# Optimization experiments

Measured on AMD Instinct MI355X. Metric: run time of the kernel, lower is better.

The kernel has to match this reference:

```python
import jax, jax.numpy as jnp
import numpy as np

# Dims: tokens [B,H,W,C]; 3x3 local window (NB=9 neighbors); relative-pos embed dim RP.
B, H, W, C = 4, 96, 96, 128
K, NB, RP = 3, 9, 8
HID = 128              # edge_hidden_dim = max(hidden_dim//2=128, feature_dim=128)
EDGE_IN = 3 * C + RP   # [center, neighbor, center-neighbor, rel_pos] -> 392
CLIP = 3.0
GATE_EPS = 1e-6
LN_EPS = 1e-5


def _ln(x, w, b):
    m = jnp.mean(x, axis=-1, keepdims=True)
    v = jnp.mean((x - m) ** 2, axis=-1, keepdims=True)
    return (x - m) * jax.lax.rsqrt(v + LN_EPS) * w + b


def _mlp(x, w1, b1, w2, b2):
    # Linear -> GELU (exact/erf, torch default) -> Linear; dropout is identity in eval mode.
    return jax.nn.gelu(x @ w1 + b1, approximate=False) @ w2 + b2


def _eml(drive, resistance, gamma_raw, lam, bias, warmup_eta):
    # EMLUnit energy gate (source not provided; Ohm's-law style drive/resistance,
    # positive resistance via softplus, clipped, warmup-scaled, learned bias).
    gamma = jax.nn.softplus(gamma_raw)
    conduct = drive / (jax.nn.softplus(resistance) + gamma + GATE_EPS)
    return warmup_eta * jnp.clip(lam * conduct, -CLIP, CLIP) + bias


def setup_inputs() -> dict:
    key = jax.random.key(0)
    ks = jax.random.split(key, 8)

    def w(k, shape, std=0.01):
        return jax.random.normal(k, shape, jnp.float32) * std

    return {
        "tokens": jax.random.normal(ks[0], (B, H, W, C), jnp.float32),
        "ln1_w": jnp.ones((C,), jnp.float32), "ln1_b": jnp.zeros((C,), jnp.float32),
        "ln2_w": jnp.ones((C,), jnp.float32), "ln2_b": jnp.zeros((C,), jnp.float32),
        "rel_pos": w(ks[1], (NB, RP), 0.02),
        "d_w1": w(ks[2], (EDGE_IN, HID)), "d_b1": jnp.zeros((HID,), jnp.float32),
        "d_w2": w(ks[3], (HID, 1)), "d_b2": jnp.zeros((1,), jnp.float32),
        "r_w1": w(ks[4], (EDGE_IN, HID)), "r_b1": jnp.zeros((HID,), jnp.float32),
        "r_w2": w(ks[5], (HID, 1)), "r_b2": jnp.zeros((1,), jnp.float32),
        "v_w": w(ks[6], (C, C)), "v_b": jnp.zeros((C,), jnp.float32),
        "o_w": w(ks[7], (C, C)), "o_b": jnp.zeros((C,), jnp.float32),
        "eml_gamma": jnp.full((1,), 0.1, jnp.float32),
        "eml_lam": jnp.ones((1,), jnp.float32),
        "eml_bias": jnp.full((1,), -0.3, jnp.float32),
    }


def reference(tokens, ln1_w, ln1_b, ln2_w, ln2_b, rel_pos,
              d_w1, d_b1, d_w2, d_b2, r_w1, r_b1, r_w2, r_b2,
              v_w, v_b, o_w, o_b, eml_gamma, eml_lam, eml_bias):
    b, h, w_, c = tokens.shape
    hw = h * w_
    norm = _ln(tokens, ln1_w, ln1_b)
    # nn.Unfold(kernel=3, padding=1): zero-pad then gather 3x3 windows (row-major ky,kx order).
    pad = jnp.pad(norm, ((0, 0), (1, 1), (1, 1), (0, 0)))
    neigh = jnp.stack([pad[:, dy:dy + h, dx:dx + w_, :]
                       for dy in range(K) for dx in range(K)], axis=3)  # [B,H,W,9,C]
    neigh = neigh.reshape(b, hw, NB, c)
    center = jnp.broadcast_to(norm.reshape(b, hw, 1, c), (b, hw, NB, c))
    relp = jnp.broadcast_to(rel_pos[None, None], (b, hw, NB, RP))
    edge = jnp.concatenate([center, neigh, center - neigh, relp], axis=-1)  # [B,HW,9,392]
    drive = _mlp(edge, d_w1, d_b1, d_w2, d_b2)[..., 0]        # [B,HW,9]
    resistance = _mlp(edge, r_w1, r_b1, r_w2, r_b2)[..., 0]   # [B,HW,9]
    energy = _eml(drive, resistance, eml_gamma, eml_lam, eml_bias, 1.0)
    gate = jax.nn.sigmoid(energy)[..., None]                  # [B,HW,9,1]
    values = neigh @ v_w + v_b                                # [B,HW,9,C]
    gate_mass = jnp.clip(jnp.sum(gate, axis=2), GATE_EPS, None)  # [B,HW,1]
    message = jnp.sum(gate * values, axis=2) / gate_mass      # [B,HW,C]
    update = (message @ o_w + o_b).reshape(b, h, w_, c)
    return _ln(tokens + update, ln2_w, ln2_b)
```

## Files before the change

### kernel.cpp

```cpp
#include <hip/hip_runtime.h>
#include <stdint.h>

#define NPIX 36864

using bf16x8 = __attribute__((ext_vector_type(8))) short;
using f32x4  = __attribute__((ext_vector_type(4))) float;
using f32x2  = __attribute__((ext_vector_type(2))) float;

__device__ __forceinline__ float bf2f(uint16_t u){
  return __uint_as_float(((uint32_t)u) << 16);
}
__device__ __forceinline__ float bl(uint32_t u){ return __uint_as_float(u << 16); }
__device__ __forceinline__ float bh(uint32_t u){ return __uint_as_float(u & 0xFFFF0000u); }
__device__ __forceinline__ uint16_t f2bf(float f){
  uint32_t u = __float_as_uint(f);
  u += 0x7fffu + ((u >> 16) & 1u);
  return (uint16_t)(u >> 16);
}
__device__ __forceinline__ float ldw(const void* p, int i, bool f32){
  return f32 ? ((const float*)p)[i] : bf2f(((const uint16_t*)p)[i]);
}
__device__ __forceinline__ bool probe_f32(const void* ones_vec){
  return ((const uint32_t*)ones_vec)[0] == 0x3F800000u;
}
__device__ __forceinline__ float softplusf(float x){
  return fmaxf(x, 0.f) + __logf(1.f + __expf(-fabsf(x)));
}
__device__ __forceinline__ f32x2 up2(uint32_t u){
  f32x2 r; r.x = __uint_as_float(u << 16); r.y = __uint_as_float(u & 0xFFFF0000u); return r;
}
__device__ __forceinline__ void sg2(f32x2& acc, uint32_t c, uint32_t n, f32x2 r, f32x2 w){
  f32x2 z = up2(c) + up2(n) + r;
  f32x2 t = z * (-1.702f);
  f32x2 e; e.x = __expf(t.x); e.y = __expf(t.y);
  f32x2 den = e + 1.0f;
  f32x2 s; s.x = __builtin_amdgcn_rcpf(den.x); s.y = __builtin_amdgcn_rcpf(den.y);
  acc += z * s * w;
}

__global__ __launch_bounds__(256) void pre_kernel(const void* __restrict__ tokens,
                            const void* __restrict__ ln1w, const void* __restrict__ ln1b,
                            const void* __restrict__ dw1, const void* __restrict__ rw1,
                            const void* __restrict__ vw,  const void* __restrict__ relp,
                            const void* __restrict__ db1, const void* __restrict__ rb1,
                            const void* __restrict__ ow,
                            const void* __restrict__ dw2, const void* __restrict__ rw2,
                            const void* __restrict__ vb,  const void* __restrict__ db2,
                            const void* __restrict__ rb2, const void* __restrict__ eg,
                            const void* __restrict__ el,  const void* __restrict__ eb,
                            uint16_t* __restrict__ norm,
                            uint16_t* __restrict__ wcatT, float* __restrict__ Rd,
                            float* __restrict__ Rr, uint16_t* __restrict__ owT,
                            float* __restrict__ w2df, float* __restrict__ w2rf,
                            float* __restrict__ vbf, float* __restrict__ sc){
  const bool F = probe_f32(ln1w);
  const int b = blockIdx.x;
  if (b < NPIX/4){
    const int wv = threadIdx.x >> 6, lane = threadIdx.x & 63;
    const int p = b * 4 + wv;
    float f0, f1;
    if (F){
      const float2 t = ((const float2*)tokens)[(size_t)p*64 + lane];
      f0 = t.x; f1 = t.y;
    } else {
      const uint32_t pk = ((const uint32_t*)tokens)[(size_t)p*64 + lane];
      f0 = bl(pk); f1 = bh(pk);
    }
    float s = f0 + f1;
    #pragma unroll
    for (int m = 1; m < 64; m <<= 1) s += __shfl_xor(s, m, 64);
    const float mean = s * (1.f/128.f);
    const float d0 = f0 - mean, d1 = f1 - mean;
    float q = d0*d0 + d1*d1;
    #pragma unroll
    for (int m = 1; m < 64; m <<= 1) q += __shfl_xor(q, m, 64);
    const float rs = rsqrtf(q * (1.f/128.f) + 1e-5f);
    const float n0 = d0*rs*ldw(ln1w, 2*lane, F)   + ldw(ln1b, 2*lane, F);
    const float n1 = d1*rs*ldw(ln1w, 2*lane+1, F) + ldw(ln1b, 2*lane+1, F);
    ((uint32_t*)(norm + (size_t)p*128))[lane] = (uint32_t)f2bf(n0) | ((uint32_t)f2bf(n1) << 16);
    return;
  }
  const int j = (b - NPIX/4) * 2 + (threadIdx.x >> 7);
  const int c = threadIdx.x & 127;
  if (j < 640){
    float val;
    if (j < 128)      val = ldw(dw1, c*128 + j, F)             + ldw(dw1, (256+c)*128 + j, F);
    else if (j < 256) val = ldw(dw1, (128+c)*128 + (j-128), F) - ldw(dw1, (256+c)*128 + (j-128), F);
    else if (j < 384) val = ldw(rw1, c*128 + (j-256), F)       + ldw(rw1, (256+c)*128 + (j-256), F);
    else if (j < 512) val = ldw(rw1, (128+c)*128 + (j-384), F) - ldw(rw1, (256+c)*128 + (j-384), F);
    else              val = ldw(vw, c*128 + (j-512), F);
    wcatT[j*128 + c] = f2bf(val);
  } else if (j < 649){
    const int k = j - 640;
    float sd = ldw(db1, c, F);
    float sr = ldw(rb1, c, F);
    #pragma unroll
    for (int r = 0; r < 8; ++r){
      float rp = ldw(relp, k*8 + r, F);
      sd += rp * ldw(dw1, (384+r)*128 + c, F);
      sr += rp * ldw(rw1, (384+r)*128 + c, F);
    }
    Rd[k*128 + c] = sd;
    Rr[k*128 + c] = sr;
  } else if (j < 777){
    const int n = j - 649;
    owT[n*128 + c] = f2bf(ldw(ow, c*128 + n, F));
  } else {
    w2df[c] = ldw(dw2, c, F);
    w2rf[c] = ldw(rw2, c, F);
    vbf[c]  = ldw(vb, c, F);
    if (c == 0){
      sc[0] = ldw(db2, 0, F);
      sc[1] = ldw(rb2, 0, F);
      sc[2] = softplusf(ldw(eg, 0, F));
      sc[3] = ldw(el, 0, F);
      sc[4] = ldw(eb, 0, F);
    }
  }
}

#define CSTRIDE 136
__global__ __launch_bounds__(256) void gemm1_kernel(const uint16_t* __restrict__ A,
                                                    const uint16_t* __restrict__ BT,
                                                    uint16_t* __restrict__ PT,
                                                    uint16_t* __restrict__ V){
  __shared__ __align__(16) char smem[65536];
  uint16_t* As = (uint16_t*)smem;
  uint16_t* Bs = (uint16_t*)(smem + 32768);
  uint16_t* Cs = (uint16_t*)smem;
  const int row0 = blockIdx.x * 128;
  const int s    = blockIdx.y;
  const int col0 = s * 128;
  const int t = threadIdx.x;
  #pragma unroll
  for (int i = 0; i < 8; ++i){
    int cid = t + i*256;
    int r = cid >> 4, c8 = cid & 15;
    int scz = c8 ^ (r & 15);
    *(uint4*)&As[r*128 + scz*8] = *(const uint4*)&A[(size_t)(row0+r)*128 + c8*8];
    *(uint4*)&Bs[r*128 + scz*8] = *(const uint4*)&BT[(size_t)(col0+r)*128 + c8*8];
  }
  __syncthreads();
  const int wv = t >> 6, lane = t & 63;
  const int wr = (wv >> 1) * 64, wc = (wv & 1) * 64;
  const int lr = lane & 15, quad = lane >> 4;
  f32x4 acc[4][4] = {};
  #pragma unroll
  for (int kk = 0; kk < 4; ++kk){
    const int chunk = kk*4 + quad;
    bf16x8 a[4], b[4];
    #pragma unroll
    for (int mi = 0; mi < 4; ++mi){
      int r = wr + mi*16 + lr;
      a[mi] = *(const bf16x8*)&As[r*128 + (chunk ^ (r & 15))*8];
    }
    #pragma unroll
    for (int ni = 0; ni < 4; ++ni){
      int r = wc + ni*16 + lr;
      b[ni] = *(const bf16x8*)&Bs[r*128 + (chunk ^ (r & 15))*8];
    }
    #pragma unroll
    for (int mi = 0; mi < 4; ++mi)
      #pragma unroll
      for (int ni = 0; ni < 4; ++ni)
        acc[mi][ni] = __builtin_amdgcn_mfma_f32_16x16x32_bf16(a[mi], b[ni], acc[mi][ni], 0, 0, 0);
  }
  __syncthreads();
  #pragma unroll
  for (int mi = 0; mi < 4; ++mi){
    #pragma unroll
    for (int ni = 0; ni < 4; ++ni){
      const int ch   = wc + ni*16 + lr;
      const int rowb = wr + mi*16 + quad*4;
      #pragma unroll
      for (int r = 0; r < 4; ++r)
        Cs[(rowb + r)*CSTRIDE + ch] = f2bf(acc[mi][ni][r]);
    }
  }
  __syncthreads();
  if (s < 4){
    #pragma unroll
    for (int i = 0; i < 8; ++i){
      const int idx = t + i*256;
      const int p = idx & 127, c = idx >> 7;
      const uint4 v = *(const uint4*)&Cs[p*CSTRIDE + c*8];
      ((uint4*)PT)[(size_t)(s*16 + c)*NPIX + (row0 + p)] = v;
    }
  } else {
    #pragma unroll
    for (int i = 0; i < 8; ++i){
      const int idx = t + i*256;
      const int c8 = idx & 15, p = idx >> 4;
      const uint4 v = *(const uint4*)&Cs[p*CSTRIDE + c8*8];
      ((uint4*)V)[(size_t)(row0 + p)*16 + c8] = v;
    }
  }
}

__global__ __launch_bounds__(192) void edge_kernel(const uint16_t* __restrict__ PTraw,
    const float* __restrict__ Rd, const float* __restrict__ Rr,
    const float* __restrict__ w2df, const float* __restrict__ w2rf,
    const float* __restrict__ sc, float* __restrict__ gates){
  const int wv = threadIdx.x >> 6, lane = threadIdx.x & 63;
  const int k = __builtin_amdgcn_readfirstlane(blockIdx.y * 3 + wv);
  const int p = blockIdx.x * 64 + lane;
  const int dy = k/3 - 1, dx = k%3 - 1;
  const int x = p % 96, y = (p / 96) % 96;
  const bool inb = ((unsigned)(x + dx) < 96u) && ((unsigned)(y + dy) < 96u);
  const uint32_t m = inb ? 0xFFFFFFFFu : 0u;
  const int q = inb ? (p + dy*96 + dx) : p;
  const uint4* PT4 = (const uint4*)PTraw;
  const float4* rd4 = (const float4*)(Rd + k*128);
  const float4* rr4 = (const float4*)(Rr + k*128);
  const float4* wd4 = (const float4*)w2df;
  const float4* wr4 = (const float4*)w2rf;
  const float sc0 = sc[0], sc1 = sc[1], sc2 = sc[2], sc3 = sc[3], sc4 = sc[4];
  f32x2 ad = {0.f, 0.f}, ar = {0.f, 0.f};
  uint4 cd = PT4[(size_t)( 0)*NPIX + p];
  uint4 nd = PT4[(size_t)(16)*NPIX + q];
  uint4 cr = PT4[(size_t)(32)*NPIX + p];
  uint4 nr = PT4[(size_t)(48)*NPIX + q];
  #pragma unroll
  for (int i = 0; i < 16; ++i){
    uint4 cdn, ndn, crn, nrn;
    if (i < 15){
      cdn = PT4[(size_t)( 0 + i+1)*NPIX + p];
      ndn = PT4[(size_t)(16 + i+1)*NPIX + q];
      crn = PT4[(size_t)(32 + i+1)*NPIX + p];
      nrn = PT4[(size_t)(48 + i+1)*NPIX + q];
    }
    nd.x &= m; nd.y &= m; nd.z &= m; nd.w &= m;
    nr.x &= m; nr.y &= m; nr.z &= m; nr.w &= m;
    const float4 rdA = rd4[2*i], rdB = rd4[2*i+1];
    const float4 rrA = rr4[2*i], rrB = rr4[2*i+1];
    const float4 wdA = wd4[2*i], wdB = wd4[2*i+1];
    const float4 wrA = wr4[2*i], wrB = wr4[2*i+1];
    sg2(ad, cd.x, nd.x, f32x2{rdA.x, rdA.y}, f32x2{wdA.x, wdA.y});
    sg2(ad, cd.y, nd.y, f32x2{rdA.z, rdA.w}, f32x2{wdA.z, wdA.w});
    sg2(ad, cd.z, nd.z, f32x2{rdB.x, rdB.y}, f32x2{wdB.x, wdB.y});
    sg2(ad, cd.w, nd.w, f32x2{rdB.z, rdB.w}, f32x2{wdB.z, wdB.w});
    sg2(ar, cr.x, nr.x, f32x2{rrA.x, rrA.y}, f32x2{wrA.x, wrA.y});
    sg2(ar, cr.y, nr.y, f32x2{rrA.z, rrA.w}, f32x2{wrA.z, wrA.w});
    sg2(ar, cr.z, nr.z, f32x2{rrB.x, rrB.y}, f32x2{wrB.x, wrB.y});
    sg2(ar, cr.w, nr.w, f32x2{rrB.z, rrB.w}, f32x2{wrB.z, wrB.w});
    cd = cdn; nd = ndn; cr = crn; nr = nrn;
  }
  const float drive  = (ad.x + ad.y) + sc0;
  const float resist = (ar.x + ar.y) + sc1;
  const float cond = __fdividef(drive, softplusf(resist) + sc2 + 1e-6f);
  const float en = fminf(fmaxf(sc3 * cond, -3.0f), 3.0f) + sc4;
  const float e = __expf(-en);
  const float g = __builtin_amdgcn_rcpf(1.0f + e);
  gates[(size_t)k*NPIX + p] = g;
}

__global__ __launch_bounds__(256) void msg_kernel(const uint16_t* __restrict__ V,
    const float* __restrict__ gates, const float* __restrict__ vbf,
    uint16_t* __restrict__ msg){
  const int wv = __builtin_amdgcn_readfirstlane(threadIdx.x >> 6);
  const int lane = threadIdx.x & 63;
  const int p = blockIdx.x * 4 + wv;
  const int x = p % 96, y = (p / 96) % 96;
  float g[9], gsum = 0.f;
  #pragma unroll
  for (int k = 0; k < 9; ++k){ g[k] = gates[(size_t)k*NPIX + p]; gsum += g[k]; }
  float a0 = 0.f, a1 = 0.f;
  #pragma unroll
  for (int k = 0; k < 9; ++k){
    const int dy = k/3 - 1, dx = k%3 - 1;
    if (((unsigned)(y + dy) < 96u) && ((unsigned)(x + dx) < 96u)){
      const uint32_t u = ((const uint32_t*)(V + (size_t)(p + dy*96 + dx)*128))[lane];
      a0 = fmaf(g[k], bl(u), a0);
      a1 = fmaf(g[k], bh(u), a1);
    }
  }
  const float2 vb2 = ((const float2*)vbf)[lane];
  const float inv = __fdividef(1.0f, fmaxf(gsum, 1e-6f));
  a0 = (a0 + gsum * vb2.x) * inv;
  a1 = (a1 + gsum * vb2.y) * inv;
  ((uint32_t*)(msg + (size_t)p*128))[lane] = (uint32_t)f2bf(a0) | ((uint32_t)f2bf(a1) << 16);
}

__global__ __launch_bounds__(256) void out_kernel(const uint16_t* __restrict__ Amsg,
    const uint16_t* __restrict__ owT, const void* __restrict__ tokens,
    const void* __restrict__ ob,  const void* __restrict__ ln2w,
    const void* __restrict__ ln2b, void* __restrict__ out){
  const bool F = probe_f32(ln2w);
  __shared__ __align__(16) char smem[65536];
  uint16_t* As = (uint16_t*)smem;
  uint16_t* Bs = (uint16_t*)(smem + 32768);
  float*    U  = (float*)smem;
  const int row0 = blockIdx.x * 128;
  const int t = threadIdx.x;
  #pragma unroll
  for (int i = 0; i < 8; ++i){
    int cid = t + i*256;
    int r = cid >> 4, c8 = cid & 15;
    int scz = c8 ^ (r & 15);
    *(uint4*)&As[r*128 + scz*8] = *(const uint4*)&Amsg[(size_t)(row0+r)*128 + c8*8];
    *(uint4*)&Bs[r*128 + scz*8] = *(const uint4*)&owT[(size_t)r*128 + c8*8];
  }
  __syncthreads();
  const int wv = t >> 6, lane = t & 63;
  const int wr = (wv >> 1) * 64, wc = (wv & 1) * 64;
  const int lr = lane & 15, quad = lane >> 4;
  f32x4 acc[4][4] = {};
  #pragma unroll
  for (int kk = 0; kk < 4; ++kk){
    const int chunk = kk*4 + quad;
    bf16x8 a[4], b[4];
    #pragma unroll
    for (int mi = 0; mi < 4; ++mi){
      int r = wr + mi*16 + lr;
      a[mi] = *(const bf16x8*)&As[r*128 + (chunk ^ (r & 15))*8];
    }
    #pragma unroll
    for (int ni = 0; ni < 4; ++ni){
      int r = wc + ni*16 + lr;
      b[ni] = *(const bf16x8*)&Bs[r*128 + (chunk ^ (r & 15))*8];
    }
    #pragma unroll
    for (int mi = 0; mi < 4; ++mi)
      #pragma unroll
      for (int ni = 0; ni < 4; ++ni)
        acc[mi][ni] = __builtin_amdgcn_mfma_f32_16x16x32_bf16(a[mi], b[ni], acc[mi][ni], 0, 0, 0);
  }
  __syncthreads();
  #pragma unroll
  for (int mi = 0; mi < 4; ++mi)
    #pragma unroll
    for (int ni = 0; ni < 4; ++ni)
      #pragma unroll
      for (int r = 0; r < 4; ++r)
        U[(wr + mi*16 + quad*4 + r)*128 + (wc + ni*16 + lr)] = acc[mi][ni][r];
  __syncthreads();
  const float lw0 = ldw(ln2w, 2*lane, F), lw1 = ldw(ln2w, 2*lane+1, F);
  const float lb0 = ldw(ln2b, 2*lane, F), lb1 = ldw(ln2b, 2*lane+1, F);
  const float ob0 = ldw(ob, 2*lane, F),   ob1 = ldw(ob, 2*lane+1, F);
  for (int rr = 0; rr < 32; ++rr){
    const int row = wv*32 + rr;
    const int p = row0 + row;
    const float2 uv = ((const float2*)U)[row*64 + lane];
    float t0, t1;
    if (F){
      const float2 tk = ((const float2*)tokens)[(size_t)p*64 + lane];
      t0 = tk.x; t1 = tk.y;
    } else {
      const uint32_t tk = ((const uint32_t*)tokens)[(size_t)p*64 + lane];
      t0 = bl(tk); t1 = bh(tk);
    }
    const float a0 = uv.x + ob0 + t0;
    const float a1 = uv.y + ob1 + t1;
    float s = a0 + a1;
    #pragma unroll
    for (int m = 1; m < 64; m <<= 1) s += __shfl_xor(s, m, 64);
    const float mean = s * (1.f/128.f);
    const float d0 = a0 - mean, d1 = a1 - mean;
    float q = d0*d0 + d1*d1;
    #pragma unroll
    for (int m = 1; m < 64; m <<= 1) q += __shfl_xor(q, m, 64);
    const float rs = rsqrtf(q * (1.f/128.f) + 1e-5f);
    const float o0 = d0*rs*lw0 + lb0;
    const float o1 = d1*rs*lw1 + lb1;
    if (F){
      ((float2*)out)[(size_t)p*64 + lane] = make_float2(o0, o1);
    } else {
      ((uint32_t*)out)[(size_t)p*64 + lane] = (uint32_t)f2bf(o0) | ((uint32_t)f2bf(o1) << 16);
    }
  }
}

extern "C" void kernel_launch(void* const* d_in, const int* in_sizes, int n_in,
                              void* d_out, int out_size, void* d_ws, size_t ws_size,
                              hipStream_t stream) {
  const void* tokens = d_in[0];
  const void* ln1w   = d_in[1];
  const void* ln1b   = d_in[2];
  const void* ln2w   = d_in[3];
  const void* ln2b   = d_in[4];
  const void* relp   = d_in[5];
  const void* dw1    = d_in[6];
  const void* db1    = d_in[7];
  const void* dw2    = d_in[8];
  const void* db2    = d_in[9];
  const void* rw1    = d_in[10];
  const void* rb1    = d_in[11];
  const void* rw2    = d_in[12];
  const void* rb2    = d_in[13];
  const void* vw     = d_in[14];
  const void* vb     = d_in[15];
  const void* ow     = d_in[16];
  const void* ob     = d_in[17];
  const void* eg     = d_in[18];
  const void* el     = d_in[19];
  const void* eb     = d_in[20];

  char* ws = (char*)d_ws;
  uint16_t* normb = (uint16_t*)(ws + 0);
  uint16_t* PT    = (uint16_t*)(ws + 9437184);
  uint16_t* V     = (uint16_t*)(ws + 47185920);
  float*    gates = (float*)   (ws + 56623104);
  uint16_t* wcatT = (uint16_t*)(ws + 57950208);
  float*    Rd    = (float*)   (ws + 58114048);
  float*    Rr    = (float*)   (ws + 58118656);
  uint16_t* owT   = (uint16_t*)(ws + 58123264);
  float*    w2df  = (float*)   (ws + 58156032);
  float*    w2rf  = (float*)   (ws + 58156544);
  float*    vbf   = (float*)   (ws + 58157056);
  float*    sc    = (float*)   (ws + 58157568);
  uint16_t* msg   = normb;

  pre_kernel<<<NPIX/4 + 389, 256, 0, stream>>>(tokens, ln1w, ln1b,
                                       dw1, rw1, vw, relp, db1, rb1, ow,
                                       dw2, rw2, vb, db2, rb2, eg, el, eb,
                                       normb, wcatT, Rd, Rr, owT, w2df, w2rf, vbf, sc);
  gemm1_kernel<<<dim3(NPIX/128, 5), 256, 0, stream>>>(normb, wcatT, PT, V);
  edge_kernel<<<dim3(NPIX/64, 3), 192, 0, stream>>>(PT, Rd, Rr, w2df, w2rf, sc, gates);
  msg_kernel<<<NPIX/4, 256, 0, stream>>>(V, gates, vbf, msg);
  out_kernel<<<NPIX/128, 256, 0, stream>>>(msg, owT, tokens, ob, ln2w, ln2b, d_out);
}
```

Baseline: 210.3 us.

## Fuse LayerNorm into edge GEMM, fuse message gather into output GEMM

LayerNorm-1 now runs inside the first GEMM kernel, which writes normalized rows straight to shared memory and then loops over all five weight column slabs, instead of storing `norm` to global memory. The message gather is folded into the output GEMM kernel the same way, so `msg` never goes through global memory and two kernel launches disappear. The sigmoid-based GELU approximation is also swapped for an algebraic rsqrt form, with the 0.5 factor folded into the second-layer weights. In exchange, both fused kernels launch only 288 blocks and each wave processes 32 pixels one after another, which lowers parallelism and latency hiding.

```diff
diff --git a/kernel.cpp b/kernel.cpp
--- a/kernel.cpp
+++ b/kernel.cpp
@@ -31,56 +31,33 @@
 }
 __device__ __forceinline__ void sg2(f32x2& acc, uint32_t c, uint32_t n, f32x2 r, f32x2 w){
   f32x2 z = up2(c) + up2(n) + r;
-  f32x2 t = z * (-1.702f);
-  f32x2 e; e.x = __expf(t.x); e.y = __expf(t.y);
-  f32x2 den = e + 1.0f;
-  f32x2 s; s.x = __builtin_amdgcn_rcpf(den.x); s.y = __builtin_amdgcn_rcpf(den.y);
-  acc += z * s * w;
-}
-
-__global__ __launch_bounds__(256) void pre_kernel(const void* __restrict__ tokens,
-                            const void* __restrict__ ln1w, const void* __restrict__ ln1b,
+  f32x2 t = z * 0.851f;
+  float rsx = rsqrtf(fmaf(t.x, t.x, 1.0f));
+  float rsy = rsqrtf(fmaf(t.y, t.y, 1.0f));
+  f32x2 zt = z * t;
+  float gx = fmaf(zt.x, rsx, z.x);
+  float gy = fmaf(zt.y, rsy, z.y);
+  acc.x = fmaf(gx, w.x, acc.x);
+  acc.y = fmaf(gy, w.y, acc.y);
+}
+
+#define LIDX(p, ch) ((p)*128 + ((((ch) >> 3) ^ ((p) & 15)) << 3) + ((ch) & 7))
+
+__global__ __launch_bounds__(256) void pre_kernel(
                             const void* __restrict__ dw1, const void* __restrict__ rw1,
                             const void* __restrict__ vw,  const void* __restrict__ relp,
                             const void* __restrict__ db1, const void* __restrict__ rb1,
-                            const void* __restrict__ ow,
+                            const void* __restrict__ ow,  const void* __restrict__ probe,
                             const void* __restrict__ dw2, const void* __restrict__ rw2,
                             const void* __restrict__ vb,  const void* __restrict__ db2,
                             const void* __restrict__ rb2, const void* __restrict__ eg,
                             const void* __restrict__ el,  const void* __restrict__ eb,
-                            uint16_t* __restrict__ norm,
                             uint16_t* __restrict__ wcatT, float* __restrict__ Rd,
                             float* __restrict__ Rr, uint16_t* __restrict__ owT,
                             float* __restrict__ w2df, float* __restrict__ w2rf,
                             float* __restrict__ vbf, float* __restrict__ sc){
-  const bool F = probe_f32(ln1w);
-  const int b = blockIdx.x;
-  if (b < NPIX/4){
-    const int wv = threadIdx.x >> 6, lane = threadIdx.x & 63;
-    const int p = b * 4 + wv;
-    float f0, f1;
-    if (F){
-      const float2 t = ((const float2*)tokens)[(size_t)p*64 + lane];
-      f0 = t.x; f1 = t.y;
-    } else {
-      const uint32_t pk = ((const uint32_t*)tokens)[(size_t)p*64 + lane];
-      f0 = bl(pk); f1 = bh(pk);
-    }
-    float s = f0 + f1;
-    #pragma unroll
-    for (int m = 1; m < 64; m <<= 1) s += __shfl_xor(s, m, 64);
-    const float mean = s * (1.f/128.f);
-    const float d0 = f0 - mean, d1 = f1 - mean;
-    float q = d0*d0 + d1*d1;
-    #pragma unroll
-    for (int m = 1; m < 64; m <<= 1) q += __shfl_xor(q, m, 64);
-    const float rs = rsqrtf(q * (1.f/128.f) + 1e-5f);
-    const float n0 = d0*rs*ldw(ln1w, 2*lane, F)   + ldw(ln1b, 2*lane, F);
-    const float n1 = d1*rs*ldw(ln1w, 2*lane+1, F) + ldw(ln1b, 2*lane+1, F);
-    ((uint32_t*)(norm + (size_t)p*128))[lane] = (uint32_t)f2bf(n0) | ((uint32_t)f2bf(n1) << 16);
-    return;
-  }
-  const int j = (b - NPIX/4) * 2 + (threadIdx.x >> 7);
+  const bool F = probe_f32(probe);
+  const int j = blockIdx.x * 2 + (threadIdx.x >> 7);
   const int c = threadIdx.x & 127;
   if (j < 640){
     float val;
@@ -106,8 +83,8 @@
     const int n = j - 649;
     owT[n*128 + c] = f2bf(ldw(ow, c*128 + n, F));
   } else {
-    w2df[c] = ldw(dw2, c, F);
-    w2rf[c] = ldw(rw2, c, F);
+    w2df[c] = 0.5f * ldw(dw2, c, F);
+    w2rf[c] = 0.5f * ldw(rw2, c, F);
     vbf[c]  = ldw(vb, c, F);
     if (c == 0){
       sc[0] = ldw(db2, 0, F);
@@ -119,81 +96,106 @@
   }
 }
 
-#define CSTRIDE 136
-__global__ __launch_bounds__(256) void gemm1_kernel(const uint16_t* __restrict__ A,
-                                                    const uint16_t* __restrict__ BT,
-                                                    uint16_t* __restrict__ PT,
-                                                    uint16_t* __restrict__ V){
+__global__ __launch_bounds__(256) void gemmln_kernel(const void* __restrict__ tokens,
+    const void* __restrict__ ln1w, const void* __restrict__ ln1b,
+    const uint16_t* __restrict__ BT, uint16_t* __restrict__ PT, uint16_t* __restrict__ V){
+  const bool F = probe_f32(ln1w);
   __shared__ __align__(16) char smem[65536];
   uint16_t* As = (uint16_t*)smem;
   uint16_t* Bs = (uint16_t*)(smem + 32768);
-  uint16_t* Cs = (uint16_t*)smem;
   const int row0 = blockIdx.x * 128;
-  const int s    = blockIdx.y;
-  const int col0 = s * 128;
   const int t = threadIdx.x;
-  #pragma unroll
-  for (int i = 0; i < 8; ++i){
-    int cid = t + i*256;
-    int r = cid >> 4, c8 = cid & 15;
-    int scz = c8 ^ (r & 15);
-    *(uint4*)&As[r*128 + scz*8] = *(const uint4*)&A[(size_t)(row0+r)*128 + c8*8];
-    *(uint4*)&Bs[r*128 + scz*8] = *(const uint4*)&BT[(size_t)(col0+r)*128 + c8*8];
-  }
-  __syncthreads();
   const int wv = t >> 6, lane = t & 63;
+  {
+    const float w0 = ldw(ln1w, 2*lane, F), w1 = ldw(ln1w, 2*lane+1, F);
+    const float b0 = ldw(ln1b, 2*lane, F), b1 = ldw(ln1b, 2*lane+1, F);
+    for (int j = 0; j < 32; ++j){
+      const int pl = wv*32 + j;
+      const int p = row0 + pl;
+      float f0, f1;
+      if (F){
+        const float2 tk = ((const float2*)tokens)[(size_t)p*64 + lane];
+        f0 = tk.x; f1 = tk.y;
+      } else {
+        const uint32_t pk = ((const uint32_t*)tokens)[(size_t)p*64 + lane];
+        f0 = bl(pk); f1 = bh(pk);
+      }
+      float s = f0 + f1;
+      #pragma unroll
+      for (int m = 1; m < 64; m <<= 1) s += __shfl_xor(s, m, 64);
+      const float mean = s * (1.f/128.f);
+      const float d0 = f0 - mean, d1 = f1 - mean;
+      float q = d0*d0 + d1*d1;
+      #pragma unroll
+      for (int m = 1; m < 64; m <<= 1) q += __shfl_xor(q, m, 64);
+      const float rs = rsqrtf(q * (1.f/128.f) + 1e-5f);
+      const float n0 = d0*rs*w0 + b0;
+      const float n1 = d1*rs*w1 + b1;
+      *(uint32_t*)&As[LIDX(pl, 2*lane)] = (uint32_t)f2bf(n0) | ((uint32_t)f2bf(n1) << 16);
+    }
+  }
   const int wr = (wv >> 1) * 64, wc = (wv & 1) * 64;
   const int lr = lane & 15, quad = lane >> 4;
-  f32x4 acc[4][4] = {};
-  #pragma unroll
-  for (int kk = 0; kk < 4; ++kk){
-    const int chunk = kk*4 + quad;
-    bf16x8 a[4], b[4];
+  for (int s = 0; s < 5; ++s){
+    #pragma unroll
+    for (int i = 0; i < 8; ++i){
+      const int cid = t + i*256;
+      const int r = cid >> 4, c8 = cid & 15;
+      *(uint4*)&Bs[r*128 + ((c8 ^ (r & 15)) << 3)] = *(const uint4*)&BT[(size_t)(s*128 + r)*128 + c8*8];
+    }
+    __syncthreads();
+    f32x4 acc[4][4] = {};
+    #pragma unroll
+    for (int kk = 0; kk < 4; ++kk){
+      const int chunk = kk*4 + quad;
+      bf16x8 a[4], b[4];
+      #pragma unroll
+      for (int mi = 0; mi < 4; ++mi){
+        const int r = wr + mi*16 + lr;
+        a[mi] = *(const bf16x8*)&As[r*128 + ((chunk ^ (r & 15)) << 3)];
+      }
+      #pragma unroll
+      for (int ni = 0; ni < 4; ++ni){
+        const int r = wc + ni*16 + lr;
+        b[ni] = *(const bf16x8*)&Bs[r*128 + ((chunk ^ (r & 15)) << 3)];
+      }
+      #pragma unroll
+      for (int mi = 0; mi < 4; ++mi)
+        #pragma unroll
+        for (int ni = 0; ni < 4; ++ni)
+          acc[mi][ni] = __builtin_amdgcn_mfma_f32_16x16x32_bf16(a[mi], b[ni], acc[mi][ni], 0, 0, 0);
+    }
+    __syncthreads();
     #pragma unroll
     for (int mi = 0; mi < 4; ++mi){
-      int r = wr + mi*16 + lr;
-      a[mi] = *(const bf16x8*)&As[r*128 + (chunk ^ (r & 15))*8];
-    }
-    #pragma unroll
-    for (int ni = 0; ni < 4; ++ni){
-      int r = wc + ni*16 + lr;
-      b[ni] = *(const bf16x8*)&Bs[r*128 + (chunk ^ (r & 15))*8];
-    }
-    #pragma unroll
-    for (int mi = 0; mi < 4; ++mi)
-      #pragma unroll
-      for (int ni = 0; ni < 4; ++ni)
-        acc[mi][ni] = __builtin_amdgcn_mfma_f32_16x16x32_bf16(a[mi], b[ni], acc[mi][ni], 0, 0, 0);
-  }
-  __syncthreads();
-  #pragma unroll
-  for (int mi = 0; mi < 4; ++mi){
-    #pragma unroll
-    for (int ni = 0; ni < 4; ++ni){
-      const int ch   = wc + ni*16 + lr;
-      const int rowb = wr + mi*16 + quad*4;
-      #pragma unroll
-      for (int r = 0; r < 4; ++r)
-        Cs[(rowb + r)*CSTRIDE + ch] = f2bf(acc[mi][ni][r]);
-    }
-  }
-  __syncthreads();
-  if (s < 4){
-    #pragma unroll
-    for (int i = 0; i < 8; ++i){
-      const int idx = t + i*256;
-      const int p = idx & 127, c = idx >> 7;
-      const uint4 v = *(const uint4*)&Cs[p*CSTRIDE + c*8];
-      ((uint4*)PT)[(size_t)(s*16 + c)*NPIX + (row0 + p)] = v;
-    }
-  } else {
-    #pragma unroll
-    for (int i = 0; i < 8; ++i){
-      const int idx = t + i*256;
-      const int c8 = idx & 15, p = idx >> 4;
-      const uint4 v = *(const uint4*)&Cs[p*CSTRIDE + c8*8];
-      ((uint4*)V)[(size_t)(row0 + p)*16 + c8] = v;
-    }
+      #pragma unroll
+      for (int ni = 0; ni < 4; ++ni){
+        const int ch = wc + ni*16 + lr;
+        const int rowb = wr + mi*16 + quad*4;
+        #pragma unroll
+        for (int r = 0; r < 4; ++r)
+          Bs[LIDX(rowb + r, ch)] = f2bf(acc[mi][ni][r]);
+      }
+    }
+    __syncthreads();
+    if (s < 4){
+      #pragma unroll
+      for (int i = 0; i < 8; ++i){
+        const int idx = t + i*256;
+        const int p = idx & 127, c = idx >> 7;
+        const uint4 v = *(const uint4*)&Bs[p*128 + ((c ^ (p & 15)) << 3)];
+        ((uint4*)PT)[(size_t)(s*16 + c)*NPIX + (row0 + p)] = v;
+      }
+    } else {
+      #pragma unroll
+      for (int i = 0; i < 8; ++i){
+        const int idx = t + i*256;
+        const int c8 = idx & 15, p = idx >> 4;
+        const uint4 v = *(const uint4*)&Bs[p*128 + ((c8 ^ (p & 15)) << 3)];
+        ((uint4*)V)[(size_t)(row0 + p)*16 + c8] = v;
+      }
+    }
+    __syncthreads();
   }
 }
 
@@ -254,36 +256,10 @@
   gates[(size_t)k*NPIX + p] = g;
 }
 
-__global__ __launch_bounds__(256) void msg_kernel(const uint16_t* __restrict__ V,
+__global__ __launch_bounds__(256) void msgout_kernel(const uint16_t* __restrict__ V,
     const float* __restrict__ gates, const float* __restrict__ vbf,
-    uint16_t* __restrict__ msg){
-  const int wv = __builtin_amdgcn_readfirstlane(threadIdx.x >> 6);
-  const int lane = threadIdx.x & 63;
-  const int p = blockIdx.x * 4 + wv;
-  const int x = p % 96, y = (p / 96) % 96;
-  float g[9], gsum = 0.f;
-  #pragma unroll
-  for (int k = 0; k < 9; ++k){ g[k] = gates[(size_t)k*NPIX + p]; gsum += g[k]; }
-  float a0 = 0.f, a1 = 0.f;
-  #pragma unroll
-  for (int k = 0; k < 9; ++k){
-    const int dy = k/3 - 1, dx = k%3 - 1;
-    if (((unsigned)(y + dy) < 96u) && ((unsigned)(x + dx) < 96u)){
-      const uint32_t u = ((const uint32_t*)(V + (size_t)(p + dy*96 + dx)*128))[lane];
-      a0 = fmaf(g[k], bl(u), a0);
-      a1 = fmaf(g[k], bh(u), a1);
-    }
-  }
-  const float2 vb2 = ((const float2*)vbf)[lane];
-  const float inv = __fdividef(1.0f, fmaxf(gsum, 1e-6f));
-  a0 = (a0 + gsum * vb2.x) * inv;
-  a1 = (a1 + gsum * vb2.y) * inv;
-  ((uint32_t*)(msg + (size_t)p*128))[lane] = (uint32_t)f2bf(a0) | ((uint32_t)f2bf(a1) << 16);
-}
-
-__global__ __launch_bounds__(256) void out_kernel(const uint16_t* __restrict__ Amsg,
     const uint16_t* __restrict__ owT, const void* __restrict__ tokens,
-    const void* __restrict__ ob,  const void* __restrict__ ln2w,
+    const void* __restrict__ ob, const void* __restrict__ ln2w,
     const void* __restrict__ ln2b, void* __restrict__ out){
   const bool F = probe_f32(ln2w);
   __shared__ __align__(16) char smem[65536];
@@ -292,16 +268,39 @@
   float*    U  = (float*)smem;
   const int row0 = blockIdx.x * 128;
   const int t = threadIdx.x;
+  const int wv = t >> 6, lane = t & 63;
   #pragma unroll
   for (int i = 0; i < 8; ++i){
-    int cid = t + i*256;
-    int r = cid >> 4, c8 = cid & 15;
-    int scz = c8 ^ (r & 15);
-    *(uint4*)&As[r*128 + scz*8] = *(const uint4*)&Amsg[(size_t)(row0+r)*128 + c8*8];
-    *(uint4*)&Bs[r*128 + scz*8] = *(const uint4*)&owT[(size_t)r*128 + c8*8];
+    const int cid = t + i*256;
+    const int r = cid >> 4, c8 = cid & 15;
+    *(uint4*)&Bs[r*128 + ((c8 ^ (r & 15)) << 3)] = *(const uint4*)&owT[(size_t)r*128 + c8*8];
+  }
+  {
+    const float2 vb2 = ((const float2*)vbf)[lane];
+    for (int j = 0; j < 32; ++j){
+      const int pl = wv*32 + j;
+      const int p = row0 + pl;
+      const int x = p % 96, y = (p / 96) % 96;
+      float g[9], gsum = 0.f;
+      #pragma unroll
+      for (int k = 0; k < 9; ++k){ g[k] = gates[(size_t)k*NPIX + p]; gsum += g[k]; }
+      float a0 = 0.f, a1 = 0.f;
+      #pragma unroll
+      for (int k = 0; k < 9; ++k){
+        const int dy = k/3 - 1, dx = k%3 - 1;
+        if (((unsigned)(y + dy) < 96u) && ((unsigned)(x + dx) < 96u)){
+          const uint32_t u = ((const uint32_t*)V)[(size_t)(p + dy*96 + dx)*64 + lane];
+          a0 = fmaf(g[k], bl(u), a0);
+          a1 = fmaf(g[k], bh(u), a1);
+        }
+      }
+      const float inv = __fdividef(1.0f, fmaxf(gsum, 1e-6f));
+      a0 = (a0 + gsum * vb2.x) * inv;
+      a1 = (a1 + gsum * vb2.y) * inv;
+      *(uint32_t*)&As[LIDX(pl, 2*lane)] = (uint32_t)f2bf(a0) | ((uint32_t)f2bf(a1) << 16);
+    }
   }
   __syncthreads();
-  const int wv = t >> 6, lane = t & 63;
   const int wr = (wv >> 1) * 64, wc = (wv & 1) * 64;
   const int lr = lane & 15, quad = lane >> 4;
   f32x4 acc[4][4] = {};
@@ -311,13 +310,13 @@
     bf16x8 a[4], b[4];
     #pragma unroll
     for (int mi = 0; mi < 4; ++mi){
-      int r = wr + mi*16 + lr;
-      a[mi] = *(const bf16x8*)&As[r*128 + (chunk ^ (r & 15))*8];
+      const int r = wr + mi*16 + lr;
+      a[mi] = *(const bf16x8*)&As[r*128 + ((chunk ^ (r & 15)) << 3)];
     }
     #pragma unroll
     for (int ni = 0; ni < 4; ++ni){
-      int r = wc + ni*16 + lr;
-      b[ni] = *(const bf16x8*)&Bs[r*128 + (chunk ^ (r & 15))*8];
+      const int r = wc + ni*16 + lr;
+      b[ni] = *(const bf16x8*)&Bs[r*128 + ((chunk ^ (r & 15)) << 3)];
     }
     #pragma unroll
     for (int mi = 0; mi < 4; ++mi)
@@ -396,26 +395,22 @@
   const void* eb     = d_in[20];
 
   char* ws = (char*)d_ws;
-  uint16_t* normb = (uint16_t*)(ws + 0);
-  uint16_t* PT    = (uint16_t*)(ws + 9437184);
-  uint16_t* V     = (uint16_t*)(ws + 47185920);
-  float*    gates = (float*)   (ws + 56623104);
-  uint16_t* wcatT = (uint16_t*)(ws + 57950208);
-  float*    Rd    = (float*)   (ws + 58114048);
-  float*    Rr    = (float*)   (ws + 58118656);
-  uint16_t* owT   = (uint16_t*)(ws + 58123264);
-  float*    w2df  = (float*)   (ws + 58156032);
-  float*    w2rf  = (float*)   (ws + 58156544);
-  float*    vbf   = (float*)   (ws + 58157056);
-  float*    sc    = (float*)   (ws + 58157568);
-  uint16_t* msg   = normb;
-
-  pre_kernel<<<NPIX/4 + 389, 256, 0, stream>>>(tokens, ln1w, ln1b,
-                                       dw1, rw1, vw, relp, db1, rb1, ow,
-                                       dw2, rw2, vb, db2, rb2, eg, el, eb,
-                                       normb, wcatT, Rd, Rr, owT, w2df, w2rf, vbf, sc);
-  gemm1_kernel<<<dim3(NPIX/128, 5), 256, 0, stream>>>(normb, wcatT, PT, V);
+  uint16_t* PT    = (uint16_t*)(ws + 0);
+  uint16_t* V     = (uint16_t*)(ws + 37748736);
+  float*    gates = (float*)   (ws + 47185920);
+  uint16_t* wcatT = (uint16_t*)(ws + 48513024);
+  float*    Rd    = (float*)   (ws + 48676864);
+  float*    Rr    = (float*)   (ws + 48681472);
+  uint16_t* owT   = (uint16_t*)(ws + 48686080);
+  float*    w2df  = (float*)   (ws + 48718848);
+  float*    w2rf  = (float*)   (ws + 48719360);
+  float*    vbf   = (float*)   (ws + 48719872);
+  float*    sc    = (float*)   (ws + 48720384);
+
+  pre_kernel<<<389, 256, 0, stream>>>(dw1, rw1, vw, relp, db1, rb1, ow, ln1w,
+                                      dw2, rw2, vb, db2, rb2, eg, el, eb,
+                                      wcatT, Rd, Rr, owT, w2df, w2rf, vbf, sc);
+  gemmln_kernel<<<NPIX/128, 256, 0, stream>>>(tokens, ln1w, ln1b, wcatT, PT, V);
   edge_kernel<<<dim3(NPIX/64, 3), 192, 0, stream>>>(PT, Rd, Rr, w2df, w2rf, sc, gates);
-  msg_kernel<<<NPIX/4, 256, 0, stream>>>(V, gates, vbf, msg);
-  out_kernel<<<NPIX/128, 256, 0, stream>>>(msg, owT, tokens, ob, ln2w, ln2b, d_out);
-}
+  msgout_kernel<<<NPIX/128, 256, 0, stream>>>(V, gates, vbf, owT, tokens, ob, ln2w, ln2b, d_out);
+}
```

New measurement: 404.5 us. 1.92x slower.

## Fuse gated message aggregation into the output projection and LayerNorm kernel

Applied to the files above, without the earlier changes.

Merges msg_kernel and out_kernel into one kernel. Each block computes the gated neighbor messages for 64 pixels directly into swizzled LDS, then runs the 128x128 output projection with MFMA and the residual+LayerNorm epilogue. This drops a kernel launch and the global round trip of the bf16 message tensor. In exchange each block reloads the full owT weight, and the tile is smaller (64 rows, one wave per 16 rows), so there is less MFMA reuse per block.

```diff
diff --git a/kernel.cpp b/kernel.cpp
--- a/kernel.cpp
+++ b/kernel.cpp
@@ -37,6 +37,8 @@
   f32x2 s; s.x = __builtin_amdgcn_rcpf(den.x); s.y = __builtin_amdgcn_rcpf(den.y);
   acc += z * s * w;
 }
+
+#define LIDX(p, ch) ((p)*128 + ((((ch) >> 3) ^ ((p) & 15)) << 3) + ((ch) & 7))
 
 __global__ __launch_bounds__(256) void pre_kernel(const void* __restrict__ tokens,
                             const void* __restrict__ ln1w, const void* __restrict__ ln1b,
@@ -152,12 +154,12 @@
     #pragma unroll
     for (int mi = 0; mi < 4; ++mi){
       int r = wr + mi*16 + lr;
-      a[mi] = *(const bf16x8*)&As[r*128 + (chunk ^ (r & 15))*8];
+      a[mi] = *(const bf16x8*)&As[r*128 + ((chunk ^ (r & 15)) << 3)];
     }
     #pragma unroll
     for (int ni = 0; ni < 4; ++ni){
       int r = wc + ni*16 + lr;
-      b[ni] = *(const bf16x8*)&Bs[r*128 + (chunk ^ (r & 15))*8];
+      b[ni] = *(const bf16x8*)&Bs[r*128 + ((chunk ^ (r & 15)) << 3)];
     }
     #pragma unroll
     for (int mi = 0; mi < 4; ++mi)
@@ -254,93 +256,77 @@
   gates[(size_t)k*NPIX + p] = g;
 }
 
-__global__ __launch_bounds__(256) void msg_kernel(const uint16_t* __restrict__ V,
+__global__ __launch_bounds__(256) void msgout_kernel(const uint16_t* __restrict__ V,
     const float* __restrict__ gates, const float* __restrict__ vbf,
-    uint16_t* __restrict__ msg){
-  const int wv = __builtin_amdgcn_readfirstlane(threadIdx.x >> 6);
-  const int lane = threadIdx.x & 63;
-  const int p = blockIdx.x * 4 + wv;
-  const int x = p % 96, y = (p / 96) % 96;
-  float g[9], gsum = 0.f;
-  #pragma unroll
-  for (int k = 0; k < 9; ++k){ g[k] = gates[(size_t)k*NPIX + p]; gsum += g[k]; }
-  float a0 = 0.f, a1 = 0.f;
-  #pragma unroll
-  for (int k = 0; k < 9; ++k){
-    const int dy = k/3 - 1, dx = k%3 - 1;
-    if (((unsigned)(y + dy) < 96u) && ((unsigned)(x + dx) < 96u)){
-      const uint32_t u = ((const uint32_t*)(V + (size_t)(p + dy*96 + dx)*128))[lane];
-      a0 = fmaf(g[k], bl(u), a0);
-      a1 = fmaf(g[k], bh(u), a1);
-    }
-  }
-  const float2 vb2 = ((const float2*)vbf)[lane];
-  const float inv = __fdividef(1.0f, fmaxf(gsum, 1e-6f));
-  a0 = (a0 + gsum * vb2.x) * inv;
-  a1 = (a1 + gsum * vb2.y) * inv;
-  ((uint32_t*)(msg + (size_t)p*128))[lane] = (uint32_t)f2bf(a0) | ((uint32_t)f2bf(a1) << 16);
-}
-
-__global__ __launch_bounds__(256) void out_kernel(const uint16_t* __restrict__ Amsg,
     const uint16_t* __restrict__ owT, const void* __restrict__ tokens,
-    const void* __restrict__ ob,  const void* __restrict__ ln2w,
+    const void* __restrict__ ob, const void* __restrict__ ln2w,
     const void* __restrict__ ln2b, void* __restrict__ out){
   const bool F = probe_f32(ln2w);
-  __shared__ __align__(16) char smem[65536];
-  uint16_t* As = (uint16_t*)smem;
-  uint16_t* Bs = (uint16_t*)(smem + 32768);
-  float*    U  = (float*)smem;
-  const int row0 = blockIdx.x * 128;
+  __shared__ __align__(16) char smem[49152];
+  uint16_t* Bs = (uint16_t*)smem;
+  uint16_t* As = (uint16_t*)(smem + 32768);
+  const int row0 = blockIdx.x * 64;
   const int t = threadIdx.x;
+  const int wv = t >> 6, lane = t & 63;
   #pragma unroll
   for (int i = 0; i < 8; ++i){
-    int cid = t + i*256;
-    int r = cid >> 4, c8 = cid & 15;
-    int scz = c8 ^ (r & 15);
-    *(uint4*)&As[r*128 + scz*8] = *(const uint4*)&Amsg[(size_t)(row0+r)*128 + c8*8];
-    *(uint4*)&Bs[r*128 + scz*8] = *(const uint4*)&owT[(size_t)r*128 + c8*8];
+    const int cid = t + i*256;
+    const int r = cid >> 4, c8 = cid & 15;
+    *(uint4*)&Bs[r*128 + ((c8 ^ (r & 15)) << 3)] = *(const uint4*)&owT[(size_t)r*128 + c8*8];
+  }
+  {
+    const float2 vb2 = ((const float2*)vbf)[lane];
+    for (int j = 0; j < 16; ++j){
+      const int pl = wv*16 + j;
+      const int p = row0 + pl;
+      const int x = p % 96, y = (p / 96) % 96;
+      float g[9], gsum = 0.f;
+      #pragma unroll
+      for (int k = 0; k < 9; ++k){ g[k] = gates[(size_t)k*NPIX + p]; gsum += g[k]; }
+      float a0 = 0.f, a1 = 0.f;
+      #pragma unroll
+      for (int k = 0; k < 9; ++k){
+        const int dy = k/3 - 1, dx = k%3 - 1;
+        if (((unsigned)(y + dy) < 96u) && ((unsigned)(x + dx) < 96u)){
+          const uint32_t u = ((const uint32_t*)V)[(size_t)(p + dy*96 + dx)*64 + lane];
+          a0 = fmaf(g[k], bl(u), a0);
+          a1 = fmaf(g[k], bh(u), a1);
+        }
+      }
+      const float inv = __fdividef(1.0f, fmaxf(gsum, 1e-6f));
+      a0 = (a0 + gsum * vb2.x) * inv;
+      a1 = (a1 + gsum * vb2.y) * inv;
+      *(uint32_t*)&As[LIDX(pl, 2*lane)] = (uint32_t)f2bf(a0) | ((uint32_t)f2bf(a1) << 16);
+    }
   }
   __syncthreads();
-  const int wv = t >> 6, lane = t & 63;
-  const int wr = (wv >> 1) * 64, wc = (wv & 1) * 64;
   const int lr = lane & 15, quad = lane >> 4;
-  f32x4 acc[4][4] = {};
+  f32x4 acc[8] = {};
   #pragma unroll
   for (int kk = 0; kk < 4; ++kk){
     const int chunk = kk*4 + quad;
-    bf16x8 a[4], b[4];
-    #pragma unroll
-    for (int mi = 0; mi < 4; ++mi){
-      int r = wr + mi*16 + lr;
-      a[mi] = *(const bf16x8*)&As[r*128 + (chunk ^ (r & 15))*8];
-    }
-    #pragma unroll
-    for (int ni = 0; ni < 4; ++ni){
-      int r = wc + ni*16 + lr;
-      b[ni] = *(const bf16x8*)&Bs[r*128 + (chunk ^ (r & 15))*8];
-    }
-    #pragma unroll
-    for (int mi = 0; mi < 4; ++mi)
-      #pragma unroll
-      for (int ni = 0; ni < 4; ++ni)
-        acc[mi][ni] = __builtin_amdgcn_mfma_f32_16x16x32_bf16(a[mi], b[ni], acc[mi][ni], 0, 0, 0);
+    const int ra = wv*16 + lr;
+    const bf16x8 a = *(const bf16x8*)&As[ra*128 + ((chunk ^ (ra & 15)) << 3)];
+    #pragma unroll
+    for (int ni = 0; ni < 8; ++ni){
+      const int rb = ni*16 + lr;
+      const bf16x8 b = *(const bf16x8*)&Bs[rb*128 + ((chunk ^ (rb & 15)) << 3)];
+      acc[ni] = __builtin_amdgcn_mfma_f32_16x16x32_bf16(a, b, acc[ni], 0, 0, 0);
+    }
   }
   __syncthreads();
-  #pragma unroll
-  for (int mi = 0; mi < 4; ++mi)
-    #pragma unroll
-    for (int ni = 0; ni < 4; ++ni)
-      #pragma unroll
-      for (int r = 0; r < 4; ++r)
-        U[(wr + mi*16 + quad*4 + r)*128 + (wc + ni*16 + lr)] = acc[mi][ni][r];
-  __syncthreads();
+  float* U = (float*)(smem + wv*8192);
+  #pragma unroll
+  for (int ni = 0; ni < 8; ++ni)
+    #pragma unroll
+    for (int r = 0; r < 4; ++r)
+      U[(quad*4 + r)*128 + ni*16 + lr] = acc[ni][r];
   const float lw0 = ldw(ln2w, 2*lane, F), lw1 = ldw(ln2w, 2*lane+1, F);
   const float lb0 = ldw(ln2b, 2*lane, F), lb1 = ldw(ln2b, 2*lane+1, F);
   const float ob0 = ldw(ob, 2*lane, F),   ob1 = ldw(ob, 2*lane+1, F);
-  for (int rr = 0; rr < 32; ++rr){
-    const int row = wv*32 + rr;
-    const int p = row0 + row;
-    const float2 uv = ((const float2*)U)[row*64 + lane];
+  for (int j = 0; j < 16; ++j){
+    const int p = row0 + wv*16 + j;
+    const float2 uv = ((const float2*)U)[j*64 + lane];
     float t0, t1;
     if (F){
       const float2 tk = ((const float2*)tokens)[(size_t)p*64 + lane];
@@ -408,7 +394,6 @@
   float*    w2rf  = (float*)   (ws + 58156544);
   float*    vbf   = (float*)   (ws + 58157056);
   float*    sc    = (float*)   (ws + 58157568);
-  uint16_t* msg   = normb;
 
   pre_kernel<<<NPIX/4 + 389, 256, 0, stream>>>(tokens, ln1w, ln1b,
                                        dw1, rw1, vw, relp, db1, rb1, ow,
@@ -416,6 +401,5 @@
                                        normb, wcatT, Rd, Rr, owT, w2df, w2rf, vbf, sc);
   gemm1_kernel<<<dim3(NPIX/128, 5), 256, 0, stream>>>(normb, wcatT, PT, V);
   edge_kernel<<<dim3(NPIX/64, 3), 192, 0, stream>>>(PT, Rd, Rr, w2df, w2rf, sc, gates);
-  msg_kernel<<<NPIX/4, 256, 0, stream>>>(V, gates, vbf, msg);
-  out_kernel<<<NPIX/128, 256, 0, stream>>>(msg, owT, tokens, ob, ln2w, ln2b, d_out);
-}
+  msgout_kernel<<<NPIX/64, 256, 0, stream>>>(V, gates, vbf, owT, tokens, ob, ln2w, ln2b, d_out);
+}
```

After: 221.3 us. 5.3% more time.
